# Kernel optimization log

Measured on AMD Instinct MI355X. Metric: run time of the kernel, lower is better.

Reference implementation:

```python
import jax, jax.numpy as jnp
import numpy as np

N = 50000   # nodes
E = 600000  # edges (avg degree ~12)
R = 8       # num_relations = 2 * n_speakers**2, n_speakers=2
B = 32      # num_bases = args.batch_size
GD, H1, H2 = 128, 128, 128


def setup_inputs() -> dict:
    key = jax.random.key(0)
    ks = jax.random.split(key, 16)
    w = lambda k, shape: jax.random.normal(k, shape, jnp.float32) * 0.05
    return {
        "node_features": jax.random.normal(ks[0], (N, GD), jnp.float32),
        "edge_index": jax.random.randint(ks[1], (2, E), 0, N),
        "edge_norm": jax.random.uniform(ks[2], (E,), jnp.float32),
        "edge_type": jax.random.randint(ks[3], (E,), 0, R),
        "basis": w(ks[4], (B, GD, H1)),
        "comp": w(ks[5], (R, B)),
        "root": w(ks[6], (GD, H1)),
        "bias1": jnp.zeros((H1,), jnp.float32),
        "w_key": w(ks[7], (H1, H2)),
        "b_key": jnp.zeros((H2,), jnp.float32),
        "w_query": w(ks[8], (H1, H2)),
        "b_query": jnp.zeros((H2,), jnp.float32),
        "w_value": w(ks[9], (H1, H2)),
        "b_value": jnp.zeros((H2,), jnp.float32),
        "w_skip": w(ks[10], (H1, H2)),
        "b_skip": jnp.zeros((H2,), jnp.float32),
    }


def reference(node_features, edge_index, edge_norm, edge_type, basis, comp,
              root, bias1, w_key, b_key, w_query, b_query, w_value, b_value,
              w_skip, b_skip):
    n = node_features.shape[0]
    r = comp.shape[0]
    src, dst = edge_index[0], edge_index[1]

    # ---- RGCNConv (basis decomposition, per-relation mean aggregation) ----
    W = jnp.einsum('rb,bio->rio', comp, basis)            # [R, GD, H1]
    xW = jnp.einsum('ni,rio->rno', node_features, W)      # [R, N, H1]
    msg = xW[edge_type, src]                              # [E, H1]
    seg = edge_type * n + dst                             # combined (relation, dst) segment id
    agg = jax.ops.segment_sum(msg, seg, num_segments=r * n).reshape(r, n, -1)
    cnt = jax.ops.segment_sum(jnp.ones(msg.shape[0], jnp.float32), seg,
                              num_segments=r * n).reshape(r, n, 1)
    h = (agg / jnp.maximum(cnt, 1.0)).sum(0) + node_features @ root + bias1

    # ---- ResGatedGraphConv: sigmoid(k_i + q_j) * v_j, sum-aggregated + skip ----
    k = h @ w_key + b_key
    q = h @ w_query + b_query
    v = h @ w_value + b_value
    m = jax.nn.sigmoid(k[dst] + q[src]) * v[src]          # [E, H2]
    out = jax.ops.segment_sum(m, dst, num_segments=n) + h @ w_skip + b_skip
    return out
```

## Files before the change

### kernel.cpp

```cpp
#include <hip/hip_runtime.h>
#include <stdint.h>

#define GD 128
#define H1 128
#define H2 128
#define NBASES 32
#define NREL 8
#define KA 1152

typedef __attribute__((ext_vector_type(8))) short bf16x8;
typedef __attribute__((ext_vector_type(4))) float f32x4;

static inline size_t align256(size_t x){ return (x + 255) & ~(size_t)255; }

__device__ __forceinline__ float bf2f(uint32_t u16){
  union { uint32_t u; float f; } c; c.u = (u16 & 0xffffu) << 16; return c.f;
}
__device__ __forceinline__ unsigned short f2bf(float f){
  union { float f; uint32_t u; } c; c.f = f;
  uint32_t u = c.u;
  u += 0x7fffu + ((u >> 16) & 1u);
  return (unsigned short)(u >> 16);
}
__device__ __forceinline__ uint32_t pkbf(float a, float b){
  union { float f; uint32_t u; } ca, cb; ca.f = a; cb.f = b;
  return __builtin_amdgcn_perm(cb.u + 0x8000u, ca.u + 0x8000u, 0x07060302u);
}

__device__ __forceinline__ void async_copy16(void* lds_dst, const void* gsrc){
  __builtin_amdgcn_global_load_lds(
      (const __attribute__((address_space(1))) uint32_t*)gsrc,
      (__attribute__((address_space(3))) uint32_t*)lds_dst, 16, 0, 0);
}

__global__ void k_prep(const float* __restrict__ comp, const float* __restrict__ basis,
                       const float* __restrict__ root, unsigned short* __restrict__ Bht,
                       const float* __restrict__ wk, const float* __restrict__ wq,
                       const float* __restrict__ wv, const float* __restrict__ wsk,
                       const float* __restrict__ bk, const float* __restrict__ bq,
                       const float* __restrict__ bv, const float* __restrict__ bs,
                       unsigned short* __restrict__ B2t, float* __restrict__ Bb,
                       const float4* __restrict__ x, uint2* __restrict__ xout, int cnt4,
                       uint32_t* __restrict__ xpadz, int npadz,
                       const int* __restrict__ edst, const int* __restrict__ etyp,
                       int* __restrict__ cnt, int E, int n){
  const float LOG2E = 1.4426950408889634f;
  int b = blockIdx.x, t = threadIdx.x;
  if (b < 128){
    int i = b;
    int o = t & 127, rh = t >> 7;
    float bv[NBASES];
    #pragma unroll
    for (int bb = 0; bb < NBASES; ++bb)
      bv[bb] = basis[((size_t)bb*GD + i)*H1 + o];
    #pragma unroll
    for (int rr = 0; rr < 4; ++rr){
      int r = rh*4 + rr;
      float acc = 0.f;
      #pragma unroll
      for (int bb = 0; bb < NBASES; ++bb)
        acc += comp[r*NBASES + bb] * bv[bb];
      Bht[(size_t)o*KA + r*128 + i] = f2bf(acc);
    }
    if (rh == 1) Bht[(size_t)o*KA + 1024 + i] = f2bf(root[(size_t)i*H1 + o]);
  } else if (b < 128 + 256){
    int idx = (b - 128)*256 + t;
    int c = idx / H1, k = idx % H1;
    const float* w = (c < 128) ? wk : (c < 256) ? wq : (c < 384) ? wv : wsk;
    float val = w[(size_t)k*H2 + (c & 127)];
    if (c < 256) val *= LOG2E;
    B2t[idx] = f2bf(val);
    if (idx < 512){
      const float* bia = (idx < 128) ? bk : (idx < 256) ? bq : (idx < 384) ? bv : bs;
      float bval = bia[idx & 127];
      if (idx < 256) bval *= LOG2E;
      Bb[idx] = bval;
    }
  } else {
    int cb = b - (128 + 256);
    int ncastb = (cnt4 + 1023) >> 10;
    if (cb < ncastb){
      int base = cb*1024 + t;
      #pragma unroll
      for (int u = 0; u < 4; ++u){
        int i = base + u*256;
        if (i < cnt4){
          float4 v = x[i];
          uint2 o; o.x = pkbf(v.x, v.y); o.y = pkbf(v.z, v.w);
          xout[i] = o;
        }
      }
    } else if (cb < ncastb + 12){
      int i = (cb - ncastb)*256 + t;
      if (i < npadz) xpadz[i] = 0u;
    } else {
      int e = (cb - ncastb - 12)*256 + t;
      if (e < E) atomicAdd(&cnt[etyp[e]*n + edst[e]], 1);
    }
  }
}

__global__ void k_scanA(const int* __restrict__ deg, int* __restrict__ off,
                        int* __restrict__ btot, int len){
  __shared__ int wsum[16];
  int t = threadIdx.x, lane = t & 63, w = t >> 6;
  int i0 = blockIdx.x*8192 + t*8;
  int v[8];
  if (i0 + 7 < len){
    int4 va = *(const int4*)(deg + i0);
    int4 vb = *(const int4*)(deg + i0 + 4);
    v[0]=va.x; v[1]=va.y; v[2]=va.z; v[3]=va.w;
    v[4]=vb.x; v[5]=vb.y; v[6]=vb.z; v[7]=vb.w;
  } else {
    #pragma unroll
    for (int u = 0; u < 8; ++u) v[u] = (i0+u < len) ? deg[i0+u] : 0;
  }
  int s[8]; s[0] = v[0];
  #pragma unroll
  for (int u = 1; u < 8; ++u) s[u] = s[u-1] + v[u];
  int x = s[7];
  #pragma unroll
  for (int d = 1; d < 64; d <<= 1){
    int u = __shfl_up(x, d, 64);
    if (lane >= d) x += u;
  }
  if (lane == 63) wsum[w] = x;
  __syncthreads();
  if (t < 16){
    int y = wsum[t];
    #pragma unroll
    for (int d = 1; d < 16; d <<= 1){
      int u = __shfl_up(y, d, 16);
      if (t >= d) y += u;
    }
    wsum[t] = y;
  }
  __syncthreads();
  int woff = (w > 0) ? wsum[w-1] : 0;
  int excl = woff + x - s[7];
  #pragma unroll
  for (int u = 0; u < 8; ++u)
    if (i0+u < len) off[i0+u] = excl + s[u] - v[u];
  if (t == 0) btot[blockIdx.x] = wsum[15];
}

__global__ void k_scanB(const int* __restrict__ btot, int* __restrict__ off,
                        int* __restrict__ cursor, int len, int sentinel){
  int t = threadIdx.x, bid = blockIdx.x;
  int add = 0;
  for (int j = 0; j < bid; ++j) add += btot[j];
  int i0 = bid*8192 + t*8;
  #pragma unroll
  for (int u = 0; u < 8; ++u){
    int i = i0 + u;
    if (i < len){ int val = off[i] + add; off[i] = val; cursor[i] = val; }
  }
  if (bid == 0 && t == 0) off[len] = sentinel;
}

__global__ void k_scatter_rd(const int* __restrict__ src, const int* __restrict__ dst,
                             const int* __restrict__ typ, int* __restrict__ cursor,
                             int* __restrict__ pk, int E, int n){
  int e = blockIdx.x*blockDim.x + threadIdx.x;
  if (e >= E) return;
  int pos = atomicAdd(&cursor[typ[e]*n + dst[e]], 1);
  pk[pos] = src[e];
}

__global__ void k_agg(const int* __restrict__ off_rd, const int* __restrict__ pk_rd,
                      const uint32_t* __restrict__ x32, unsigned short* __restrict__ A2,
                      int n, int npad){
  int wid = blockIdx.x*(blockDim.x >> 6) + (threadIdx.x >> 6);
  int lane = threadIdx.x & 63;
  if (wid >= npad) return;
  uint32_t* arow = (uint32_t*)(A2 + (size_t)wid*1024);
  if (wid >= n){
    #pragma unroll
    for (int u = 0; u < 8; ++u) arow[u*64 + lane] = 0u;
    return;
  }
  int r8 = lane & 7;
  int o_r = off_rd[(size_t)r8*n + wid];
  int e_r = off_rd[(size_t)r8*n + wid + 1];
  int c_r = e_r - o_r;
  float ic_r = (c_r > 0) ? __builtin_amdgcn_rcpf((float)c_r) : 0.f;
  int c0_ = __builtin_amdgcn_readlane(c_r, 0), c1_ = __builtin_amdgcn_readlane(c_r, 1);
  int c2_ = __builtin_amdgcn_readlane(c_r, 2), c3_ = __builtin_amdgcn_readlane(c_r, 3);
  int c4_ = __builtin_amdgcn_readlane(c_r, 4), c5_ = __builtin_amdgcn_readlane(c_r, 5);
  int c6_ = __builtin_amdgcn_readlane(c_r, 6), c7_ = __builtin_amdgcn_readlane(c_r, 7);
  int o0_ = __builtin_amdgcn_readlane(o_r, 0), o1_ = __builtin_amdgcn_readlane(o_r, 1);
  int o2_ = __builtin_amdgcn_readlane(o_r, 2), o3_ = __builtin_amdgcn_readlane(o_r, 3);
  int o4_ = __builtin_amdgcn_readlane(o_r, 4), o5_ = __builtin_amdgcn_readlane(o_r, 5);
  int o6_ = __builtin_amdgcn_readlane(o_r, 6), o7_ = __builtin_amdgcn_readlane(o_r, 7);
  int p1 = c0_, p2 = p1 + c1_, p3 = p2 + c2_, p4 = p3 + c3_;
  int p5 = p4 + c4_, p6 = p5 + c5_, p7 = p6 + c6_, dg = p7 + c7_;

  int cr = 0;
  float a0 = 0.f, a1 = 0.f;

#define FLUSH(RK)                                                               \
  {                                                                             \
    float ic = __int_as_float(__builtin_amdgcn_readlane(__float_as_int(ic_r), cr)); \
    arow[cr*64 + lane] = pkbf(a0*ic, a1*ic);                                    \
    for (int q = cr + 1; q < (RK); ++q) arow[q*64 + lane] = 0u;                 \
    cr = (RK); a0 = 0.f; a1 = 0.f;                                              \
  }

  for (int jb = 0; jb < dg; jb += 64){
    int i = jb + lane;
    int adj = o0_, rel = 0;
    adj = (i >= p1) ? (o1_ - p1) : adj;  rel += (i >= p1);
    adj = (i >= p2) ? (o2_ - p2) : adj;  rel += (i >= p2);
    adj = (i >= p3) ? (o3_ - p3) : adj;  rel += (i >= p3);
    adj = (i >= p4) ? (o4_ - p4) : adj;  rel += (i >= p4);
    adj = (i >= p5) ? (o5_ - p5) : adj;  rel += (i >= p5);
    adj = (i >= p6) ? (o6_ - p6) : adj;  rel += (i >= p6);
    adj = (i >= p7) ? (o7_ - p7) : adj;  rel += (i >= p7);
    int m = dg - jb; if (m > 64) m = 64;
    int pj = (lane < m) ? pk_rd[adj + i] : 0;
    int jj = 0;
    for (; jj + 8 <= m; jj += 8){
      uint32_t g[8];
      #pragma unroll
      for (int k = 0; k < 8; ++k){
        int sN = __builtin_amdgcn_readlane(pj, jj + k);
        g[k] = x32[(size_t)(uint32_t)sN*64 + lane];
      }
      #pragma unroll
      for (int k = 0; k < 8; ++k){
        int rk = __builtin_amdgcn_readlane(rel, jj + k);
        if (rk != cr) FLUSH(rk);
        a0 += bf2f(g[k]); a1 += bf2f(g[k] >> 16);
      }
    }
    for (; jj < m; jj += 4){
      int lim = m - 1;
      uint32_t g[4];
      #pragma unroll
      for (int k = 0; k < 4; ++k){
        int tt = jj + k; if (tt > lim) tt = lim;
        int sN = __builtin_amdgcn_readlane(pj, tt);
        g[k] = x32[(size_t)(uint32_t)sN*64 + lane];
      }
      #pragma unroll
      for (int k = 0; k < 4; ++k){
        int tt = jj + k;
        if (tt < m){
          int rk = __builtin_amdgcn_readlane(rel, tt);
          if (rk != cr) FLUSH(rk);
          a0 += bf2f(g[k]); a1 += bf2f(g[k] >> 16);
        }
      }
    }
  }
  FLUSH(8)
#undef FLUSH
}

__launch_bounds__(256)
__global__ void k_hgemm(const unsigned short* __restrict__ A, const unsigned short* __restrict__ xb,
                        const unsigned short* __restrict__ Bt,
                        const float* __restrict__ bias1, unsigned short* __restrict__ h){
  __shared__ char lds[16896];
  int t = threadIdx.x, lane = t & 63, wave = t >> 6;
  int row0 = blockIdx.x * 128;
  int mrow = lane & 15, quad = lane >> 4;
  int wrow = (wave & 1) * 64, wcol = (wave >> 1) * 64;
  int s = (mrow >> 1) & 3;
  int colsw = (((t & 3) ^ ((t >> 3) & 3)) << 3);

  const unsigned short* Asrc = A  + (size_t)(row0 + (t >> 2))*1024 + colsw;
  const unsigned short* Xsrc = xb + (size_t)(row0 + (t >> 2))*GD   + colsw;
  const unsigned short* Bsrc = Bt + (size_t)(t >> 2)*KA + colsw;
  char* ldsw = lds + wave*1024;

  int aoff = (wrow + mrow)*64 + ((quad ^ s) << 4);
  int boff = 8192 + (wcol + mrow)*64 + ((quad ^ s) << 4);

  f32x4 acc[4][4];
  #pragma unroll
  for (int i = 0; i < 4; ++i)
    #pragma unroll
    for (int j = 0; j < 4; ++j) acc[i][j] = (f32x4){0.f,0.f,0.f,0.f};

  for (int kt = 0; kt < KA; kt += 32){
    const unsigned short* a0p = (kt < 1024) ? (Asrc + kt)
                                            : (Xsrc + (kt - 1024));
    const unsigned short* a1p = (kt < 1024) ? (Asrc + (size_t)64*1024 + kt)
                                            : (Xsrc + (size_t)64*GD + (kt - 1024));
    __syncthreads();
    async_copy16(ldsw,         a0p);
    async_copy16(ldsw + 4096,  a1p);
    async_copy16(ldsw + 8192,  Bsrc + kt);
    async_copy16(ldsw + 12288, Bsrc + (size_t)64*KA + kt);
    __syncthreads();
    bf16x8 af[4], bf[4];
    #pragma unroll
    for (int i = 0; i < 4; ++i) af[i] = *(const bf16x8*)(lds + aoff + i*1024);
    #pragma unroll
    for (int j = 0; j < 4; ++j) bf[j] = *(const bf16x8*)(lds + boff + j*1024);
    #pragma unroll
    for (int i = 0; i < 4; ++i)
      #pragma unroll
      for (int j = 0; j < 4; ++j)
        acc[i][j] = __builtin_amdgcn_mfma_f32_16x16x32_bf16(af[i], bf[j], acc[i][j], 0, 0, 0);
  }
  float bc[4];
  #pragma unroll
  for (int j = 0; j < 4; ++j) bc[j] = bias1[wcol + j*16 + mrow];
  #pragma unroll
  for (int p = 0; p < 2; ++p){
    __syncthreads();
    if ((wave & 1) == p){
      #pragma unroll
      for (int j = 0; j < 4; ++j){
        int col = wcol + j*16 + mrow;
        #pragma unroll
        for (int i = 0; i < 4; ++i)
          #pragma unroll
          for (int rg = 0; rg < 4; ++rg){
            int rl = i*16 + quad*4 + rg;
            *(unsigned short*)(lds + rl*264 + col*2) = f2bf(acc[i][j][rg] + bc[j]);
          }
      }
    }
    __syncthreads();
    uint32_t vv[16];
    #pragma unroll
    for (int u = 0; u < 8; ++u)
      *(uint2*)&vv[u*2] = *(const uint2*)(lds + lane*264 + wave*64 + u*8);
    unsigned short* gp = h + (size_t)(row0 + p*64 + lane)*H1 + wave*32;
    #pragma unroll
    for (int u = 0; u < 4; ++u)
      *(uint4*)(gp + u*8) = *(const uint4*)&vv[u*4];
  }
}

__launch_bounds__(256)
__global__ void k_gemm2(const unsigned short* __restrict__ A, const unsigned short* __restrict__ Bt,
                        const float* __restrict__ Bb, unsigned short* __restrict__ kqv,
                        unsigned short* __restrict__ skipb){
  __shared__ char lds[16896];
  int t = threadIdx.x, lane = t & 63, wave = t >> 6;
  int row0 = blockIdx.x * 128;
  int c0 = blockIdx.y * 128;
  int mrow = lane & 15, quad = lane >> 4;
  int wrow = (wave & 1) * 64, wcol = (wave >> 1) * 64;
  int s = (mrow >> 1) & 3;

  const unsigned short* Asrc = A + (size_t)(row0 + (t >> 2))*H1 + (((t & 3) ^ ((t >> 3) & 3)) << 3);
  const unsigned short* Bsrc = Bt + (size_t)(c0 + (t >> 2))*H1 + (((t & 3) ^ ((t >> 3) & 3)) << 3);
  char* ldsw = lds + wave*1024;

  int aoff = (wrow + mrow)*64 + ((quad ^ s) << 4);
  int boff = 8192 + (wcol + mrow)*64 + ((quad ^ s) << 4);

  f32x4 acc[4][4];
  #pragma unroll
  for (int i = 0; i < 4; ++i)
    #pragma unroll
    for (int j = 0; j < 4; ++j) acc[i][j] = (f32x4){0.f,0.f,0.f,0.f};

  #pragma unroll
  for (int kt = 0; kt < H1; kt += 32){
    __syncthreads();
    async_copy16(ldsw,         Asrc + kt);
    async_copy16(ldsw + 4096,  Asrc + (size_t)64*H1 + kt);
    async_copy16(ldsw + 8192,  Bsrc + kt);
    async_copy16(ldsw + 12288, Bsrc + (size_t)64*H1 + kt);
    __syncthreads();
    bf16x8 af[4], bf[4];
    #pragma unroll
    for (int i = 0; i < 4; ++i) af[i] = *(const bf16x8*)(lds + aoff + i*1024);
    #pragma unroll
    for (int j = 0; j < 4; ++j) bf[j] = *(const bf16x8*)(lds + boff + j*1024);
    #pragma unroll
    for (int i = 0; i < 4; ++i)
      #pragma unroll
      for (int j = 0; j < 4; ++j)
        acc[i][j] = __builtin_amdgcn_mfma_f32_16x16x32_bf16(af[i], bf[j], acc[i][j], 0, 0, 0);
  }
  float bc[4];
  #pragma unroll
  for (int j = 0; j < 4; ++j) bc[j] = Bb[c0 + wcol + j*16 + mrow];
  unsigned short* dstb; size_t ldu;
  if (c0 < 384){ dstb = kqv + c0; ldu = 384; } else { dstb = skipb; ldu = 128; }
  #pragma unroll
  for (int p = 0; p < 2; ++p){
    __syncthreads();
    if ((wave & 1) == p){
      #pragma unroll
      for (int j = 0; j < 4; ++j){
        int col = wcol + j*16 + mrow;
        #pragma unroll
        for (int i = 0; i < 4; ++i)
          #pragma unroll
          for (int rg = 0; rg < 4; ++rg){
            int rl = i*16 + quad*4 + rg;
            *(unsigned short*)(lds + rl*264 + col*2) = f2bf(acc[i][j][rg] + bc[j]);
          }
      }
    }
    __syncthreads();
    uint32_t vv[16];
    #pragma unroll
    for (int u = 0; u < 8; ++u)
      *(uint2*)&vv[u*2] = *(const uint2*)(lds + lane*264 + wave*64 + u*8);
    unsigned short* gp = dstb + (size_t)(row0 + p*64 + lane)*ldu + wave*32;
    #pragma unroll
    for (int u = 0; u < 4; ++u)
      *(uint4*)(gp + u*8) = *(const uint4*)&vv[u*4];
  }
}

__global__ void k_edge2(const int* __restrict__ off_rd, const int* __restrict__ pk_rd,
                        const unsigned short* __restrict__ kqv,
                        const unsigned short* __restrict__ skipb,
                        float* __restrict__ out, int n){
  int wid = blockIdx.x*(blockDim.x >> 6) + (threadIdx.x >> 6);
  int lane = threadIdx.x & 63;
  if (wid >= n) return;
  const uint32_t* kv32 = (const uint32_t*)kqv;
  int r = lane & 7;
  int o_r = off_rd[(size_t)r*n + wid];
  int e_r = off_rd[(size_t)r*n + wid + 1];
  int c_r = e_r - o_r;
  int c0_ = __builtin_amdgcn_readlane(c_r, 0), c1_ = __builtin_amdgcn_readlane(c_r, 1);
  int c2_ = __builtin_amdgcn_readlane(c_r, 2), c3_ = __builtin_amdgcn_readlane(c_r, 3);
  int c4_ = __builtin_amdgcn_readlane(c_r, 4), c5_ = __builtin_amdgcn_readlane(c_r, 5);
  int c6_ = __builtin_amdgcn_readlane(c_r, 6), c7_ = __builtin_amdgcn_readlane(c_r, 7);
  int o0_ = __builtin_amdgcn_readlane(o_r, 0), o1_ = __builtin_amdgcn_readlane(o_r, 1);
  int o2_ = __builtin_amdgcn_readlane(o_r, 2), o3_ = __builtin_amdgcn_readlane(o_r, 3);
  int o4_ = __builtin_amdgcn_readlane(o_r, 4), o5_ = __builtin_amdgcn_readlane(o_r, 5);
  int o6_ = __builtin_amdgcn_readlane(o_r, 6), o7_ = __builtin_amdgcn_readlane(o_r, 7);
  int p1 = c0_, p2 = p1 + c1_, p3 = p2 + c2_, p4 = p3 + c3_;
  int p5 = p4 + c4_, p6 = p5 + c5_, p7 = p6 + c6_, dg = p7 + c7_;

  uint32_t ku = kv32[(size_t)wid*192 + lane];
  float k0 = bf2f(ku), k1 = bf2f(ku >> 16);
  float a0 = 0.f, a1 = 0.f;
  for (int jb = 0; jb < dg; jb += 64){
    int i = jb + lane;
    int adj = o0_;
    adj = (i >= p1) ? (o1_ - p1) : adj;
    adj = (i >= p2) ? (o2_ - p2) : adj;
    adj = (i >= p3) ? (o3_ - p3) : adj;
    adj = (i >= p4) ? (o4_ - p4) : adj;
    adj = (i >= p5) ? (o5_ - p5) : adj;
    adj = (i >= p6) ? (o6_ - p6) : adj;
    adj = (i >= p7) ? (o7_ - p7) : adj;
    int m = dg - jb; if (m > 64) m = 64;
    int pj = (lane < m) ? pk_rd[adj + i] : 0;
    int jj = 0;
    for (; jj + 8 <= m; jj += 8){
      uint32_t qg[8], vg[8];
      #pragma unroll
      for (int k = 0; k < 8; ++k){
        int s = __builtin_amdgcn_readlane(pj, jj + k);
        const uint32_t* rowp = kv32 + (size_t)s*192 + lane;
        qg[k] = rowp[64];
        vg[k] = rowp[128];
      }
      #pragma unroll
      for (int k = 0; k < 8; ++k){
        float qq0 = bf2f(qg[k]), qq1 = bf2f(qg[k] >> 16);
        float vv0 = bf2f(vg[k]), vv1 = bf2f(vg[k] >> 16);
        float g0 = __builtin_amdgcn_rcpf(1.f + __builtin_amdgcn_exp2f(-(k0 + qq0)));
        float g1 = __builtin_amdgcn_rcpf(1.f + __builtin_amdgcn_exp2f(-(k1 + qq1)));
        a0 += g0*vv0; a1 += g1*vv1;
      }
    }
    for (; jj + 4 <= m; jj += 4){
      uint32_t qg[4], vg[4];
      #pragma unroll
      for (int k = 0; k < 4; ++k){
        int s = __builtin_amdgcn_readlane(pj, jj + k);
        const uint32_t* rowp = kv32 + (size_t)s*192 + lane;
        qg[k] = rowp[64];
        vg[k] = rowp[128];
      }
      #pragma unroll
      for (int k = 0; k < 4; ++k){
        float qq0 = bf2f(qg[k]), qq1 = bf2f(qg[k] >> 16);
        float vv0 = bf2f(vg[k]), vv1 = bf2f(vg[k] >> 16);
        float g0 = __builtin_amdgcn_rcpf(1.f + __builtin_amdgcn_exp2f(-(k0 + qq0)));
        float g1 = __builtin_amdgcn_rcpf(1.f + __builtin_amdgcn_exp2f(-(k1 + qq1)));
        a0 += g0*vv0; a1 += g1*vv1;
      }
    }
    for (; jj < m; ++jj){
      int s = __builtin_amdgcn_readlane(pj, jj);
      const uint32_t* rowp = kv32 + (size_t)s*192 + lane;
      uint32_t qg = rowp[64], vg = rowp[128];
      float qq0 = bf2f(qg), qq1 = bf2f(qg >> 16);
      float vv0 = bf2f(vg), vv1 = bf2f(vg >> 16);
      float g0 = __builtin_amdgcn_rcpf(1.f + __builtin_amdgcn_exp2f(-(k0 + qq0)));
      float g1 = __builtin_amdgcn_rcpf(1.f + __builtin_amdgcn_exp2f(-(k1 + qq1)));
      a0 += g0*vv0; a1 += g1*vv1;
    }
  }
  uint32_t sk = ((const uint32_t*)skipb)[(size_t)wid*64 + lane];
  float2 cur; cur.x = a0 + bf2f(sk); cur.y = a1 + bf2f(sk >> 16);
  ((float2*)(out + (size_t)wid*H2))[lane] = cur;
}

extern "C" void kernel_launch(void* const* d_in, const int* in_sizes, int n_in,
                              void* d_out, int out_size, void* d_ws, size_t ws_size,
                              hipStream_t stream){
  const float* x     = (const float*)d_in[0];
  const int*   eidx  = (const int*)  d_in[1];
  const int*   etype = (const int*)  d_in[3];
  const float* basis = (const float*)d_in[4];
  const float* comp  = (const float*)d_in[5];
  const float* root  = (const float*)d_in[6];
  const float* bias1 = (const float*)d_in[7];
  const float* wk    = (const float*)d_in[8];
  const float* bk    = (const float*)d_in[9];
  const float* wq    = (const float*)d_in[10];
  const float* bq    = (const float*)d_in[11];
  const float* wv    = (const float*)d_in[12];
  const float* bv    = (const float*)d_in[13];
  const float* wsk   = (const float*)d_in[14];
  const float* bs    = (const float*)d_in[15];
  const int n = in_sizes[0] / GD;
  const int E = in_sizes[3];
  const int npad = (n + 127) & ~127;
  const int* esrc = eidx;
  const int* edst = eidx + E;
  float* out = (float*)d_out;

  char* w = (char*)d_ws;
  size_t off = 0;
  unsigned short* xbf  = (unsigned short*)(w + off); off = align256(off + (size_t)npad*GD*2);
  unsigned short* A2   = (unsigned short*)(w + off); off = align256(off + (size_t)npad*1024*2);
  unsigned short* Bht  = (unsigned short*)(w + off); off = align256(off + (size_t)KA*H1*2);
  unsigned short* B2t  = (unsigned short*)(w + off); off = align256(off + (size_t)512*H1*2);
  float* Bb            = (float*)(w + off);          off = align256(off + 512*4);
  unsigned short* hbuf = (unsigned short*)(w + off); off = align256(off + (size_t)npad*H1*2);
  unsigned short* kqv  = (unsigned short*)(w + off); off = align256(off + (size_t)npad*384*2);
  unsigned short* skipb= (unsigned short*)(w + off); off = align256(off + (size_t)npad*H2*2);
  int* cnt_rd          = (int*)(w + off);            off = align256(off + (size_t)(8*n+4)*4);
  int* off_rd          = (int*)(w + off);            off = align256(off + (size_t)(8*n+1)*4);
  int* cur_rd          = (int*)(w + off);            off = align256(off + (size_t)8*n*4);
  int* btot_rd         = (int*)(w + off);            off = align256(off + 64*4);
  int* pk_rd           = (int*)(w + off);            off = align256(off + (size_t)E*4);

  const int nblk_rd = (8*n + 8191) / 8192;
  const int cnt4 = n*GD/4;
  const int ncastb = (cnt4 + 1023)/1024;
  const int histb  = (E + 255)/256;
  const int npadz  = (npad - n)*GD/2;

  hipMemsetAsync(cnt_rd, 0, (size_t)8*n*4, stream);

  k_prep<<<128 + 256 + ncastb + 12 + histb, 256, 0, stream>>>(
      comp, basis, root, Bht, wk, wq, wv, wsk, bk, bq, bv, bs, B2t, Bb,
      (const float4*)x, (uint2*)xbf, cnt4,
      (uint32_t*)(xbf + (size_t)n*GD), npadz,
      edst, etype, cnt_rd, E, n);
  k_scanA<<<nblk_rd, 1024, 0, stream>>>(cnt_rd, off_rd, btot_rd, 8*n);
  k_scanB<<<nblk_rd, 1024, 0, stream>>>(btot_rd, off_rd, cur_rd, 8*n, E);
  k_scatter_rd<<<(E + 255)/256, 256, 0, stream>>>(esrc, edst, etype, cur_rd, pk_rd, E, n);
  k_agg<<<(npad + 3)/4, 256, 0, stream>>>(off_rd, pk_rd, (const uint32_t*)xbf, A2, n, npad);
  k_hgemm<<<npad/128, 256, 0, stream>>>(A2, xbf, Bht, bias1, hbuf);
  k_gemm2<<<dim3(npad/128, 4), 256, 0, stream>>>(hbuf, B2t, Bb, kqv, skipb);
  k_edge2<<<(n + 3)/4, 256, 0, stream>>>(off_rd, pk_rd, kqv, skipb, out, n);
}
```

Before: 335.5 us.

## Fuse h GEMM with key/query/value/skip GEMM, keeping h tile in LDS

Merges the two GEMM kernels into one: each block computes a 64-row tile of h (the K=1152 GEMM), stores it in LDS with an XOR swizzle, then loops over the four 128-column output chunks of the second GEMM, reading A from LDS. This removes the hbuf global write/read round trip and one kernel launch. In exchange the row tile halves to 64 (smaller per-wave MFMA tiles, more B traffic per row) and LDS use grows to about 45KB, which may lower occupancy.

After: 338.9 us. About the same (+1.0%).

```diff
diff --git a/kernel.cpp b/kernel.cpp
--- a/kernel.cpp
+++ b/kernel.cpp
@@ -258,158 +258,121 @@
 }
 
 __launch_bounds__(256)
-__global__ void k_hgemm(const unsigned short* __restrict__ A, const unsigned short* __restrict__ xb,
-                        const unsigned short* __restrict__ Bt,
-                        const float* __restrict__ bias1, unsigned short* __restrict__ h){
-  __shared__ char lds[16896];
+__global__ void k_hqkv(const unsigned short* __restrict__ A, const unsigned short* __restrict__ xb,
+                       const unsigned short* __restrict__ Bt,
+                       const unsigned short* __restrict__ B2,
+                       const float* __restrict__ bias1, const float* __restrict__ Bb,
+                       unsigned short* __restrict__ kqv, unsigned short* __restrict__ skipb){
+  __shared__ char lds[45568];
   int t = threadIdx.x, lane = t & 63, wave = t >> 6;
-  int row0 = blockIdx.x * 128;
+  int row0 = blockIdx.x * 64;
   int mrow = lane & 15, quad = lane >> 4;
-  int wrow = (wave & 1) * 64, wcol = (wave >> 1) * 64;
   int s = (mrow >> 1) & 3;
   int colsw = (((t & 3) ^ ((t >> 3) & 3)) << 3);
 
   const unsigned short* Asrc = A  + (size_t)(row0 + (t >> 2))*1024 + colsw;
   const unsigned short* Xsrc = xb + (size_t)(row0 + (t >> 2))*GD   + colsw;
   const unsigned short* Bsrc = Bt + (size_t)(t >> 2)*KA + colsw;
-  char* ldsw = lds + wave*1024;
-
-  int aoff = (wrow + mrow)*64 + ((quad ^ s) << 4);
-  int boff = 8192 + (wcol + mrow)*64 + ((quad ^ s) << 4);
-
-  f32x4 acc[4][4];
+  char* ldsB  = lds + 4096;
+  char* htile = lds + 12288;
+  char* eb    = lds + 28672;
+
+  int aoff = mrow*64 + ((quad ^ s) << 4);
+  int boff = 4096 + (wave*32 + mrow)*64 + ((quad ^ s) << 4);
+  int axor = (mrow & 7) << 4;
+
+  f32x4 acc[4][2];
   #pragma unroll
   for (int i = 0; i < 4; ++i)
     #pragma unroll
-    for (int j = 0; j < 4; ++j) acc[i][j] = (f32x4){0.f,0.f,0.f,0.f};
+    for (int j = 0; j < 2; ++j) acc[i][j] = (f32x4){0.f,0.f,0.f,0.f};
 
   for (int kt = 0; kt < KA; kt += 32){
-    const unsigned short* a0p = (kt < 1024) ? (Asrc + kt)
-                                            : (Xsrc + (kt - 1024));
-    const unsigned short* a1p = (kt < 1024) ? (Asrc + (size_t)64*1024 + kt)
-                                            : (Xsrc + (size_t)64*GD + (kt - 1024));
+    const unsigned short* ap = (kt < 1024) ? (Asrc + kt) : (Xsrc + (kt - 1024));
     __syncthreads();
-    async_copy16(ldsw,         a0p);
-    async_copy16(ldsw + 4096,  a1p);
-    async_copy16(ldsw + 8192,  Bsrc + kt);
-    async_copy16(ldsw + 12288, Bsrc + (size_t)64*KA + kt);
+    async_copy16(lds  + wave*1024, ap);
+    async_copy16(ldsB + wave*1024, Bsrc + kt);
+    async_copy16(ldsB + 4096 + wave*1024, Bsrc + (size_t)64*KA + kt);
     __syncthreads();
-    bf16x8 af[4], bf[4];
+    bf16x8 af[4], bf[2];
     #pragma unroll
     for (int i = 0; i < 4; ++i) af[i] = *(const bf16x8*)(lds + aoff + i*1024);
     #pragma unroll
-    for (int j = 0; j < 4; ++j) bf[j] = *(const bf16x8*)(lds + boff + j*1024);
+    for (int j = 0; j < 2; ++j) bf[j] = *(const bf16x8*)(lds + boff + j*1024);
     #pragma unroll
     for (int i = 0; i < 4; ++i)
       #pragma unroll
-      for (int j = 0; j < 4; ++j)
+      for (int j = 0; j < 2; ++j)
         acc[i][j] = __builtin_amdgcn_mfma_f32_16x16x32_bf16(af[i], bf[j], acc[i][j], 0, 0, 0);
   }
-  float bc[4];
-  #pragma unroll
-  for (int j = 0; j < 4; ++j) bc[j] = bias1[wcol + j*16 + mrow];
-  #pragma unroll
-  for (int p = 0; p < 2; ++p){
-    __syncthreads();
-    if ((wave & 1) == p){
-      #pragma unroll
-      for (int j = 0; j < 4; ++j){
-        int col = wcol + j*16 + mrow;
+  {
+    float bc1[2];
+    #pragma unroll
+    for (int j = 0; j < 2; ++j) bc1[j] = bias1[wave*32 + j*16 + mrow];
+    #pragma unroll
+    for (int j = 0; j < 2; ++j){
+      int col = wave*32 + j*16 + mrow;
+      #pragma unroll
+      for (int i = 0; i < 4; ++i)
         #pragma unroll
-        for (int i = 0; i < 4; ++i)
-          #pragma unroll
-          for (int rg = 0; rg < 4; ++rg){
-            int rl = i*16 + quad*4 + rg;
-            *(unsigned short*)(lds + rl*264 + col*2) = f2bf(acc[i][j][rg] + bc[j]);
-          }
-      }
+        for (int rg = 0; rg < 4; ++rg){
+          int row = i*16 + quad*4 + rg;
+          *(unsigned short*)(htile + row*256 + ((col*2) ^ ((row & 7) << 4)))
+              = f2bf(acc[i][j][rg] + bc1[j]);
+        }
+    }
+  }
+  __syncthreads();
+
+  for (int c0 = 0; c0 < 4; ++c0){
+    #pragma unroll
+    for (int i = 0; i < 4; ++i)
+      #pragma unroll
+      for (int j = 0; j < 2; ++j) acc[i][j] = (f32x4){0.f,0.f,0.f,0.f};
+    const unsigned short* B2src = B2 + (size_t)(c0*128 + (t >> 2))*H1 + colsw;
+    for (int kt = 0; kt < 128; kt += 32){
+      __syncthreads();
+      async_copy16(ldsB + wave*1024, B2src + kt);
+      async_copy16(ldsB + 4096 + wave*1024, B2src + (size_t)64*H1 + kt);
+      __syncthreads();
+      bf16x8 af[4], bf[2];
+      #pragma unroll
+      for (int i = 0; i < 4; ++i)
+        af[i] = *(const bf16x8*)(htile + (i*16 + mrow)*256 + (((kt + quad*8)*2) ^ axor));
+      #pragma unroll
+      for (int j = 0; j < 2; ++j) bf[j] = *(const bf16x8*)(lds + boff + j*1024);
+      #pragma unroll
+      for (int i = 0; i < 4; ++i)
+        #pragma unroll
+        for (int j = 0; j < 2; ++j)
+          acc[i][j] = __builtin_amdgcn_mfma_f32_16x16x32_bf16(af[i], bf[j], acc[i][j], 0, 0, 0);
+    }
+    float bc2[2];
+    #pragma unroll
+    for (int j = 0; j < 2; ++j) bc2[j] = Bb[c0*128 + wave*32 + j*16 + mrow];
+    #pragma unroll
+    for (int j = 0; j < 2; ++j){
+      int col = wave*32 + j*16 + mrow;
+      #pragma unroll
+      for (int i = 0; i < 4; ++i)
+        #pragma unroll
+        for (int rg = 0; rg < 4; ++rg){
+          int rl = i*16 + quad*4 + rg;
+          *(unsigned short*)(eb + rl*264 + col*2) = f2bf(acc[i][j][rg] + bc2[j]);
+        }
     }
     __syncthreads();
     uint32_t vv[16];
     #pragma unroll
     for (int u = 0; u < 8; ++u)
-      *(uint2*)&vv[u*2] = *(const uint2*)(lds + lane*264 + wave*64 + u*8);
-    unsigned short* gp = h + (size_t)(row0 + p*64 + lane)*H1 + wave*32;
+      *(uint2*)&vv[u*2] = *(const uint2*)(eb + lane*264 + wave*64 + u*8);
+    unsigned short* dstb; size_t ldu;
+    if (c0 < 3){ dstb = kqv + c0*128; ldu = 384; } else { dstb = skipb; ldu = 128; }
+    unsigned short* gp = dstb + (size_t)(row0 + lane)*ldu + wave*32;
     #pragma unroll
     for (int u = 0; u < 4; ++u)
       *(uint4*)(gp + u*8) = *(const uint4*)&vv[u*4];
-  }
-}
-
-__launch_bounds__(256)
-__global__ void k_gemm2(const unsigned short* __restrict__ A, const unsigned short* __restrict__ Bt,
-                        const float* __restrict__ Bb, unsigned short* __restrict__ kqv,
-                        unsigned short* __restrict__ skipb){
-  __shared__ char lds[16896];
-  int t = threadIdx.x, lane = t & 63, wave = t >> 6;
-  int row0 = blockIdx.x * 128;
-  int c0 = blockIdx.y * 128;
-  int mrow = lane & 15, quad = lane >> 4;
-  int wrow = (wave & 1) * 64, wcol = (wave >> 1) * 64;
-  int s = (mrow >> 1) & 3;
-
-  const unsigned short* Asrc = A + (size_t)(row0 + (t >> 2))*H1 + (((t & 3) ^ ((t >> 3) & 3)) << 3);
-  const unsigned short* Bsrc = Bt + (size_t)(c0 + (t >> 2))*H1 + (((t & 3) ^ ((t >> 3) & 3)) << 3);
-  char* ldsw = lds + wave*1024;
-
-  int aoff = (wrow + mrow)*64 + ((quad ^ s) << 4);
-  int boff = 8192 + (wcol + mrow)*64 + ((quad ^ s) << 4);
-
-  f32x4 acc[4][4];
-  #pragma unroll
-  for (int i = 0; i < 4; ++i)
-    #pragma unroll
-    for (int j = 0; j < 4; ++j) acc[i][j] = (f32x4){0.f,0.f,0.f,0.f};
-
-  #pragma unroll
-  for (int kt = 0; kt < H1; kt += 32){
     __syncthreads();
-    async_copy16(ldsw,         Asrc + kt);
-    async_copy16(ldsw + 4096,  Asrc + (size_t)64*H1 + kt);
-    async_copy16(ldsw + 8192,  Bsrc + kt);
-    async_copy16(ldsw + 12288, Bsrc + (size_t)64*H1 + kt);
-    __syncthreads();
-    bf16x8 af[4], bf[4];
-    #pragma unroll
-    for (int i = 0; i < 4; ++i) af[i] = *(const bf16x8*)(lds + aoff + i*1024);
-    #pragma unroll
-    for (int j = 0; j < 4; ++j) bf[j] = *(const bf16x8*)(lds + boff + j*1024);
-    #pragma unroll
-    for (int i = 0; i < 4; ++i)
-      #pragma unroll
-      for (int j = 0; j < 4; ++j)
-        acc[i][j] = __builtin_amdgcn_mfma_f32_16x16x32_bf16(af[i], bf[j], acc[i][j], 0, 0, 0);
-  }
-  float bc[4];
-  #pragma unroll
-  for (int j = 0; j < 4; ++j) bc[j] = Bb[c0 + wcol + j*16 + mrow];
-  unsigned short* dstb; size_t ldu;
-  if (c0 < 384){ dstb = kqv + c0; ldu = 384; } else { dstb = skipb; ldu = 128; }
-  #pragma unroll
-  for (int p = 0; p < 2; ++p){
-    __syncthreads();
-    if ((wave & 1) == p){
-      #pragma unroll
-      for (int j = 0; j < 4; ++j){
-        int col = wcol + j*16 + mrow;
-        #pragma unroll
-        for (int i = 0; i < 4; ++i)
-          #pragma unroll
-          for (int rg = 0; rg < 4; ++rg){
-            int rl = i*16 + quad*4 + rg;
-            *(unsigned short*)(lds + rl*264 + col*2) = f2bf(acc[i][j][rg] + bc[j]);
-          }
-      }
-    }
-    __syncthreads();
-    uint32_t vv[16];
-    #pragma unroll
-    for (int u = 0; u < 8; ++u)
-      *(uint2*)&vv[u*2] = *(const uint2*)(lds + lane*264 + wave*64 + u*8);
-    unsigned short* gp = dstb + (size_t)(row0 + p*64 + lane)*ldu + wave*32;
-    #pragma unroll
-    for (int u = 0; u < 4; ++u)
-      *(uint4*)(gp + u*8) = *(const uint4*)&vv[u*4];
   }
 }
 
@@ -536,7 +499,6 @@
   unsigned short* Bht  = (unsigned short*)(w + off); off = align256(off + (size_t)KA*H1*2);
   unsigned short* B2t  = (unsigned short*)(w + off); off = align256(off + (size_t)512*H1*2);
   float* Bb            = (float*)(w + off);          off = align256(off + 512*4);
-  unsigned short* hbuf = (unsigned short*)(w + off); off = align256(off + (size_t)npad*H1*2);
   unsigned short* kqv  = (unsigned short*)(w + off); off = align256(off + (size_t)npad*384*2);
   unsigned short* skipb= (unsigned short*)(w + off); off = align256(off + (size_t)npad*H2*2);
   int* cnt_rd          = (int*)(w + off);            off = align256(off + (size_t)(8*n+4)*4);
@@ -562,7 +524,6 @@
   k_scanB<<<nblk_rd, 1024, 0, stream>>>(btot_rd, off_rd, cur_rd, 8*n, E);
   k_scatter_rd<<<(E + 255)/256, 256, 0, stream>>>(esrc, edst, etype, cur_rd, pk_rd, E, n);
   k_agg<<<(npad + 3)/4, 256, 0, stream>>>(off_rd, pk_rd, (const uint32_t*)xbf, A2, n, npad);
-  k_hgemm<<<npad/128, 256, 0, stream>>>(A2, xbf, Bht, bias1, hbuf);
-  k_gemm2<<<dim3(npad/128, 4), 256, 0, stream>>>(hbuf, B2t, Bb, kqv, skipb);
+  k_hqkv<<<npad/64, 256, 0, stream>>>(A2, xbf, Bht, B2t, bias1, Bb, kqv, skipb);
   k_edge2<<<(n + 3)/4, 256, 0, stream>>>(off_rd, pk_rd, kqv, skipb, out, n);
 }
```

## Interleave q and v per element so edge gather uses one 8-byte load

Applied to the files above, without the earlier changes.

The kernel producing k/q/v/skip now writes q and v interleaved as packed bf16 pairs in a separate qv buffer. k and skip go to their own arrays. The q/v blocks compute two passes, holding q in registers, and write the pairs directly to global memory without LDS staging. The edge kernel then fetches q and v for each source node with a single uint2 load instead of two scattered 4-byte loads. The cost is a heavier GEMM block for q/v and uncoalesced 4-byte global stores in its epilogue.

Measured after the change: 327.5 us (median of 2 runs). -2.4%, faster.

```diff
diff --git a/kernel.cpp b/kernel.cpp
--- a/kernel.cpp
+++ b/kernel.cpp
@@ -338,89 +338,123 @@
 
 __launch_bounds__(256)
 __global__ void k_gemm2(const unsigned short* __restrict__ A, const unsigned short* __restrict__ Bt,
-                        const float* __restrict__ Bb, unsigned short* __restrict__ kqv,
-                        unsigned short* __restrict__ skipb){
+                        const float* __restrict__ Bb, unsigned short* __restrict__ kbuf,
+                        uint32_t* __restrict__ qvbuf, unsigned short* __restrict__ skipb){
   __shared__ char lds[16896];
   int t = threadIdx.x, lane = t & 63, wave = t >> 6;
   int row0 = blockIdx.x * 128;
-  int c0 = blockIdx.y * 128;
+  int y = blockIdx.y;
   int mrow = lane & 15, quad = lane >> 4;
   int wrow = (wave & 1) * 64, wcol = (wave >> 1) * 64;
   int s = (mrow >> 1) & 3;
-
-  const unsigned short* Asrc = A + (size_t)(row0 + (t >> 2))*H1 + (((t & 3) ^ ((t >> 3) & 3)) << 3);
-  const unsigned short* Bsrc = Bt + (size_t)(c0 + (t >> 2))*H1 + (((t & 3) ^ ((t >> 3) & 3)) << 3);
+  int colsw = (((t & 3) ^ ((t >> 3) & 3)) << 3);
+
+  const unsigned short* Asrc = A + (size_t)(row0 + (t >> 2))*H1 + colsw;
   char* ldsw = lds + wave*1024;
 
   int aoff = (wrow + mrow)*64 + ((quad ^ s) << 4);
   int boff = 8192 + (wcol + mrow)*64 + ((quad ^ s) << 4);
 
   f32x4 acc[4][4];
-  #pragma unroll
-  for (int i = 0; i < 4; ++i)
-    #pragma unroll
-    for (int j = 0; j < 4; ++j) acc[i][j] = (f32x4){0.f,0.f,0.f,0.f};
-
-  #pragma unroll
-  for (int kt = 0; kt < H1; kt += 32){
-    __syncthreads();
-    async_copy16(ldsw,         Asrc + kt);
-    async_copy16(ldsw + 4096,  Asrc + (size_t)64*H1 + kt);
-    async_copy16(ldsw + 8192,  Bsrc + kt);
-    async_copy16(ldsw + 12288, Bsrc + (size_t)64*H1 + kt);
-    __syncthreads();
-    bf16x8 af[4], bf[4];
-    #pragma unroll
-    for (int i = 0; i < 4; ++i) af[i] = *(const bf16x8*)(lds + aoff + i*1024);
-    #pragma unroll
-    for (int j = 0; j < 4; ++j) bf[j] = *(const bf16x8*)(lds + boff + j*1024);
+  int npass = (y == 1) ? 2 : 1;
+  uint32_t qs[4][4][2];
+
+  for (int pass = 0; pass < npass; ++pass){
+    int c0 = (y == 0) ? 0 : (y == 2) ? 3 : (1 + pass);
+    const unsigned short* Bsrc = Bt + (size_t)(c0*128 + (t >> 2))*H1 + colsw;
     #pragma unroll
     for (int i = 0; i < 4; ++i)
       #pragma unroll
-      for (int j = 0; j < 4; ++j)
-        acc[i][j] = __builtin_amdgcn_mfma_f32_16x16x32_bf16(af[i], bf[j], acc[i][j], 0, 0, 0);
-  }
-  float bc[4];
-  #pragma unroll
-  for (int j = 0; j < 4; ++j) bc[j] = Bb[c0 + wcol + j*16 + mrow];
-  unsigned short* dstb; size_t ldu;
-  if (c0 < 384){ dstb = kqv + c0; ldu = 384; } else { dstb = skipb; ldu = 128; }
-  #pragma unroll
-  for (int p = 0; p < 2; ++p){
-    __syncthreads();
-    if ((wave & 1) == p){
-      #pragma unroll
-      for (int j = 0; j < 4; ++j){
-        int col = wcol + j*16 + mrow;
+      for (int j = 0; j < 4; ++j) acc[i][j] = (f32x4){0.f,0.f,0.f,0.f};
+
+    #pragma unroll
+    for (int kt = 0; kt < H1; kt += 32){
+      __syncthreads();
+      async_copy16(ldsw,         Asrc + kt);
+      async_copy16(ldsw + 4096,  Asrc + (size_t)64*H1 + kt);
+      async_copy16(ldsw + 8192,  Bsrc + kt);
+      async_copy16(ldsw + 12288, Bsrc + (size_t)64*H1 + kt);
+      __syncthreads();
+      bf16x8 af[4], bf[4];
+      #pragma unroll
+      for (int i = 0; i < 4; ++i) af[i] = *(const bf16x8*)(lds + aoff + i*1024);
+      #pragma unroll
+      for (int j = 0; j < 4; ++j) bf[j] = *(const bf16x8*)(lds + boff + j*1024);
+      #pragma unroll
+      for (int i = 0; i < 4; ++i)
+        #pragma unroll
+        for (int j = 0; j < 4; ++j)
+          acc[i][j] = __builtin_amdgcn_mfma_f32_16x16x32_bf16(af[i], bf[j], acc[i][j], 0, 0, 0);
+    }
+
+    float bc[4];
+    #pragma unroll
+    for (int j = 0; j < 4; ++j) bc[j] = Bb[c0*128 + wcol + j*16 + mrow];
+
+    if (y == 1){
+      if (pass == 0){
         #pragma unroll
         for (int i = 0; i < 4; ++i)
           #pragma unroll
-          for (int rg = 0; rg < 4; ++rg){
-            int rl = i*16 + quad*4 + rg;
-            *(unsigned short*)(lds + rl*264 + col*2) = f2bf(acc[i][j][rg] + bc[j]);
+          for (int j = 0; j < 4; ++j){
+            qs[i][j][0] = pkbf(acc[i][j][0] + bc[j], acc[i][j][1] + bc[j]);
+            qs[i][j][1] = pkbf(acc[i][j][2] + bc[j], acc[i][j][3] + bc[j]);
           }
-      }
-    }
-    __syncthreads();
-    uint32_t vv[16];
-    #pragma unroll
-    for (int u = 0; u < 8; ++u)
-      *(uint2*)&vv[u*2] = *(const uint2*)(lds + lane*264 + wave*64 + u*8);
-    unsigned short* gp = dstb + (size_t)(row0 + p*64 + lane)*ldu + wave*32;
-    #pragma unroll
-    for (int u = 0; u < 4; ++u)
-      *(uint4*)(gp + u*8) = *(const uint4*)&vv[u*4];
+      } else {
+        #pragma unroll
+        for (int j = 0; j < 4; ++j){
+          int col = wcol + j*16 + mrow;
+          #pragma unroll
+          for (int i = 0; i < 4; ++i)
+            #pragma unroll
+            for (int rg = 0; rg < 4; ++rg){
+              int row = row0 + wrow + i*16 + quad*4 + rg;
+              uint32_t ql = (qs[i][j][rg >> 1] >> ((rg & 1)*16)) & 0xffffu;
+              uint32_t pk = ql | ((uint32_t)f2bf(acc[i][j][rg] + bc[j]) << 16);
+              qvbuf[(size_t)row*128 + col] = pk;
+            }
+        }
+      }
+    } else {
+      unsigned short* dstb = (y == 0) ? kbuf : skipb;
+      #pragma unroll
+      for (int p = 0; p < 2; ++p){
+        __syncthreads();
+        if ((wave & 1) == p){
+          #pragma unroll
+          for (int j = 0; j < 4; ++j){
+            int col = wcol + j*16 + mrow;
+            #pragma unroll
+            for (int i = 0; i < 4; ++i)
+              #pragma unroll
+              for (int rg = 0; rg < 4; ++rg){
+                int rl = i*16 + quad*4 + rg;
+                *(unsigned short*)(lds + rl*264 + col*2) = f2bf(acc[i][j][rg] + bc[j]);
+              }
+          }
+        }
+        __syncthreads();
+        uint32_t vv[16];
+        #pragma unroll
+        for (int u = 0; u < 8; ++u)
+          *(uint2*)&vv[u*2] = *(const uint2*)(lds + lane*264 + wave*64 + u*8);
+        unsigned short* gp = dstb + (size_t)(row0 + p*64 + lane)*H1 + wave*32;
+        #pragma unroll
+        for (int u = 0; u < 4; ++u)
+          *(uint4*)(gp + u*8) = *(const uint4*)&vv[u*4];
+      }
+    }
   }
 }
 
 __global__ void k_edge2(const int* __restrict__ off_rd, const int* __restrict__ pk_rd,
-                        const unsigned short* __restrict__ kqv,
+                        const unsigned short* __restrict__ kbuf,
+                        const uint32_t* __restrict__ qvbuf,
                         const unsigned short* __restrict__ skipb,
                         float* __restrict__ out, int n){
   int wid = blockIdx.x*(blockDim.x >> 6) + (threadIdx.x >> 6);
   int lane = threadIdx.x & 63;
   if (wid >= n) return;
-  const uint32_t* kv32 = (const uint32_t*)kqv;
   int r = lane & 7;
   int o_r = off_rd[(size_t)r*n + wid];
   int e_r = off_rd[(size_t)r*n + wid + 1];
@@ -436,7 +470,7 @@
   int p1 = c0_, p2 = p1 + c1_, p3 = p2 + c2_, p4 = p3 + c3_;
   int p5 = p4 + c4_, p6 = p5 + c5_, p7 = p6 + c6_, dg = p7 + c7_;
 
-  uint32_t ku = kv32[(size_t)wid*192 + lane];
+  uint32_t ku = ((const uint32_t*)kbuf)[(size_t)wid*64 + lane];
   float k0 = bf2f(ku), k1 = bf2f(ku >> 16);
   float a0 = 0.f, a1 = 0.f;
   for (int jb = 0; jb < dg; jb += 64){
@@ -453,36 +487,32 @@
     int pj = (lane < m) ? pk_rd[adj + i] : 0;
     int jj = 0;
     for (; jj + 8 <= m; jj += 8){
-      uint32_t qg[8], vg[8];
+      uint2 g[8];
       #pragma unroll
       for (int k = 0; k < 8; ++k){
         int s = __builtin_amdgcn_readlane(pj, jj + k);
-        const uint32_t* rowp = kv32 + (size_t)s*192 + lane;
-        qg[k] = rowp[64];
-        vg[k] = rowp[128];
+        g[k] = *(const uint2*)(qvbuf + (size_t)s*128 + lane*2);
       }
       #pragma unroll
       for (int k = 0; k < 8; ++k){
-        float qq0 = bf2f(qg[k]), qq1 = bf2f(qg[k] >> 16);
-        float vv0 = bf2f(vg[k]), vv1 = bf2f(vg[k] >> 16);
+        float qq0 = bf2f(g[k].x), vv0 = bf2f(g[k].x >> 16);
+        float qq1 = bf2f(g[k].y), vv1 = bf2f(g[k].y >> 16);
         float g0 = __builtin_amdgcn_rcpf(1.f + __builtin_amdgcn_exp2f(-(k0 + qq0)));
         float g1 = __builtin_amdgcn_rcpf(1.f + __builtin_amdgcn_exp2f(-(k1 + qq1)));
         a0 += g0*vv0; a1 += g1*vv1;
       }
     }
     for (; jj + 4 <= m; jj += 4){
-      uint32_t qg[4], vg[4];
+      uint2 g[4];
       #pragma unroll
       for (int k = 0; k < 4; ++k){
         int s = __builtin_amdgcn_readlane(pj, jj + k);
-        const uint32_t* rowp = kv32 + (size_t)s*192 + lane;
-        qg[k] = rowp[64];
-        vg[k] = rowp[128];
+        g[k] = *(const uint2*)(qvbuf + (size_t)s*128 + lane*2);
       }
       #pragma unroll
       for (int k = 0; k < 4; ++k){
-        float qq0 = bf2f(qg[k]), qq1 = bf2f(qg[k] >> 16);
-        float vv0 = bf2f(vg[k]), vv1 = bf2f(vg[k] >> 16);
+        float qq0 = bf2f(g[k].x), vv0 = bf2f(g[k].x >> 16);
+        float qq1 = bf2f(g[k].y), vv1 = bf2f(g[k].y >> 16);
         float g0 = __builtin_amdgcn_rcpf(1.f + __builtin_amdgcn_exp2f(-(k0 + qq0)));
         float g1 = __builtin_amdgcn_rcpf(1.f + __builtin_amdgcn_exp2f(-(k1 + qq1)));
         a0 += g0*vv0; a1 += g1*vv1;
@@ -490,10 +520,9 @@
     }
     for (; jj < m; ++jj){
       int s = __builtin_amdgcn_readlane(pj, jj);
-      const uint32_t* rowp = kv32 + (size_t)s*192 + lane;
-      uint32_t qg = rowp[64], vg = rowp[128];
-      float qq0 = bf2f(qg), qq1 = bf2f(qg >> 16);
-      float vv0 = bf2f(vg), vv1 = bf2f(vg >> 16);
+      uint2 g = *(const uint2*)(qvbuf + (size_t)s*128 + lane*2);
+      float qq0 = bf2f(g.x), vv0 = bf2f(g.x >> 16);
+      float qq1 = bf2f(g.y), vv1 = bf2f(g.y >> 16);
       float g0 = __builtin_amdgcn_rcpf(1.f + __builtin_amdgcn_exp2f(-(k0 + qq0)));
       float g1 = __builtin_amdgcn_rcpf(1.f + __builtin_amdgcn_exp2f(-(k1 + qq1)));
       a0 += g0*vv0; a1 += g1*vv1;
@@ -537,7 +566,8 @@
   unsigned short* B2t  = (unsigned short*)(w + off); off = align256(off + (size_t)512*H1*2);
   float* Bb            = (float*)(w + off);          off = align256(off + 512*4);
   unsigned short* hbuf = (unsigned short*)(w + off); off = align256(off + (size_t)npad*H1*2);
-  unsigned short* kqv  = (unsigned short*)(w + off); off = align256(off + (size_t)npad*384*2);
+  unsigned short* kbuf = (unsigned short*)(w + off); off = align256(off + (size_t)npad*H1*2);
+  uint32_t* qvbuf      = (uint32_t*)(w + off);       off = align256(off + (size_t)npad*128*4);
   unsigned short* skipb= (unsigned short*)(w + off); off = align256(off + (size_t)npad*H2*2);
   int* cnt_rd          = (int*)(w + off);            off = align256(off + (size_t)(8*n+4)*4);
   int* off_rd          = (int*)(w + off);            off = align256(off + (size_t)(8*n+1)*4);
@@ -563,6 +593,6 @@
   k_scatter_rd<<<(E + 255)/256, 256, 0, stream>>>(esrc, edst, etype, cur_rd, pk_rd, E, n);
   k_agg<<<(npad + 3)/4, 256, 0, stream>>>(off_rd, pk_rd, (const uint32_t*)xbf, A2, n, npad);
   k_hgemm<<<npad/128, 256, 0, stream>>>(A2, xbf, Bht, bias1, hbuf);
-  k_gemm2<<<dim3(npad/128, 4), 256, 0, stream>>>(hbuf, B2t, Bb, kqv, skipb);
-  k_edge2<<<(n + 3)/4, 256, 0, stream>>>(off_rd, pk_rd, kqv, skipb, out, n);
-}
+  k_gemm2<<<dim3(npad/128, 3), 256, 0, stream>>>(hbuf, B2t, Bb, kbuf, qvbuf, skipb);
+  k_edge2<<<(n + 3)/4, 256, 0, stream>>>(off_rd, pk_rd, kbuf, qvbuf, skipb, out, n);
+}
```
